# Kernel tuning notes

Measured on AMD Instinct MI355X. Metric: run time of the kernel, lower is better.

## Reference

```python
import jax, jax.numpy as jnp
import numpy as np

M, K, N, GROUP = 64, 4096, 11008, 128
NGROUPS = K // GROUP  # 32


def setup_inputs() -> dict:
    key = jax.random.key(0)
    k1, k2, k3, k4, k5 = jax.random.split(key, 5)
    x = jax.random.normal(k1, (M, K), dtype=jnp.float32)
    # packed int4 weights: 8 nibbles per int32, full 32-bit entropy
    qweight = jax.random.bits(k2, (K // 8, N), dtype=jnp.uint32).astype(jnp.int32)
    qzeros = jax.random.bits(k3, (NGROUPS, N // 8), dtype=jnp.uint32).astype(jnp.int32)
    scales = jax.random.uniform(k4, (NGROUPS, N), dtype=jnp.float32, minval=0.001, maxval=0.02)
    bias = jax.random.normal(k5, (N,), dtype=jnp.float32) * 0.01
    return {"x": x, "qweight": qweight, "qzeros": qzeros, "scales": scales, "bias": bias}


def dequantize(qweight, qzeros, scales):
    shifts = jnp.arange(8, dtype=jnp.int32) * 4  # nibble bit offsets 0..28
    # unpack weights: [K//8, N] -> [K//8, 8, N] -> [NGROUPS, GROUP, N]
    w = (jnp.right_shift(qweight[:, None, :], shifts[None, :, None]) & 15)
    w = w.reshape(-1, GROUP, qweight.shape[1])
    # unpack zeros: [NGROUPS, N//8] -> [NGROUPS, N//8, 8] -> [NGROUPS, 1, N]; GPTQ stores zero-1
    z = (jnp.right_shift(qzeros[:, :, None], shifts[None, None, :]) & 15) + 1
    z = z.reshape(z.shape[0], 1, -1)
    # scale * (q - zero), per group: [NGROUPS, GROUP, N] -> [K, N]
    W = scales[:, None, :] * (w - z).astype(scales.dtype)
    return W.reshape(-1, W.shape[2])


def reference(x, qweight, qzeros, scales, bias):
    W = dequantize(qweight, qzeros, scales)  # [K, N] fp32
    return jnp.matmul(x, W.astype(x.dtype)) + bias
```

## Files before the change

kernel.cpp:

```cpp
#include <hip/hip_runtime.h>
#include <hip/hip_bf16.h>

namespace {

constexpr int MM = 64;
constexpr int KK = 4096;
constexpr int NN = 11008;
constexpr int NZROW = NN / 8;
constexpr int BN = 128;
constexpr int KSPLIT = 8;
constexpr int KSEG = KK / KSPLIT;
constexpr int NTILES = NN / BN;
constexpr int BK = 32;
constexpr int NCH = KSEG / BK;
constexpr int GCH = 4;
constexpr int NG = NCH / GCH;
constexpr int AROWI = 68;
constexpr int ABUFI = MM * AROWI;
constexpr size_t WS_NEED = (size_t)KSPLIT * MM * NN * 4;

static_assert(NCH % GCH == 0, "groups must tile chunks");

typedef float f32x4 __attribute__((ext_vector_type(4)));
typedef short s16x8 __attribute__((ext_vector_type(8)));
typedef int   i32x4 __attribute__((ext_vector_type(4)));
typedef int   i32x2 __attribute__((ext_vector_type(2)));

__device__ __forceinline__ int pack_bf16(float a, float b) {
  union { __hip_bfloat162 h; int i; } u;
  u.h.x = __float2bfloat16(a);
  u.h.y = __float2bfloat16(b);
  return u.i;
}

__global__ __launch_bounds__(256) void prep_kernel(
    const float* __restrict__ bias, float* __restrict__ out)
{
  const int i = blockIdx.x * 256 + threadIdx.x;
  out[i] = bias[i % NN];
}

__global__ __launch_bounds__(256) void reduce_kernel(
    const float* __restrict__ ws, const float* __restrict__ bias,
    float* __restrict__ out)
{
  const int i4 = (blockIdx.x * 256 + threadIdx.x) * 4;
  f32x4 acc = *(const f32x4*)(bias + (i4 % NN));
  #pragma unroll
  for (int s = 0; s < KSPLIT; ++s)
    acc += *(const f32x4*)(ws + (size_t)s * (MM * NN) + i4);
  *(f32x4*)(out + i4) = acc;
}

template<bool ATOMIC>
__global__ __launch_bounds__(256, 4) void gptq_gemm_kernel(
    const float* __restrict__ x, const int* __restrict__ qw,
    const int* __restrict__ qz, const float* __restrict__ scales,
    float* __restrict__ out)
{
  __shared__ int As[2 * ABUFI];

  const int tid  = threadIdx.x;
  const int wave = tid >> 6;
  const int lane = tid & 63;
  const int c    = lane & 15;
  const int quad = lane >> 4;

  const int ks     = blockIdx.x & 7;
  const int ntile  = blockIdx.x >> 3;
  const int n0     = ntile * BN;
  const int kbase0 = ks * KSEG;
  const int grp0   = kbase0 >> 7;

  const int ncol = n0 + wave * 32 + c;

  const int arow0 = wave * 16 + (lane >> 5);
  const float* xp0 = x + (size_t)arow0 * KK + kbase0 + (lane & 31) * 4;

  const int* qwb = qw + ((size_t)(kbase0 >> 3) + quad) * NN + ncol;

  f32x4 acc[8];
  #pragma unroll
  for (int t = 0; t < 8; ++t) acc[t] = {0.f, 0.f, 0.f, 0.f};

  f32x4 S[8];
  int   pB0[4], pB1[4];
  float pS0[2], pS1[2];
  int   pZ0[2], pZ1[2];
  float s0, s1, C0, C1;

  auto stage_load = [&](int g) {
    const float* xp = xp0 + g * 128;
    #pragma unroll
    for (int j = 0; j < 8; ++j)
      S[j] = *(const f32x4*)(xp + (size_t)j * 2 * KK);
  };
  auto stage_write = [&](int g) {
    int* Ab = As + (g & 1) * ABUFI + arow0 * AROWI + (lane & 31) * 2;
    #pragma unroll
    for (int j = 0; j < 8; ++j) {
      i32x2 w2;
      w2.x = pack_bf16(S[j].x, S[j].y);
      w2.y = pack_bf16(S[j].z, S[j].w);
      *(i32x2*)&Ab[j * 2 * AROWI] = w2;
    }
  };
  auto pfB = [&](int i) {
    const int* qp = qwb + (size_t)i * 4 * NN;
    pB0[i & 3] = qp[0];
    pB1[i & 3] = qp[16];
  };
  auto pfS = [&](int g) {
    const int sl = g & 1;
    const float* sp = scales + (size_t)(grp0 + g) * NN + ncol;
    pS0[sl] = sp[0];
    pS1[sl] = sp[16];
    const int* zp = qz + (size_t)(grp0 + g) * NZROW + (ncol >> 3);
    pZ0[sl] = zp[0];
    pZ1[sl] = zp[2];
  };
  auto setSC = [&](int g) {
    const int sl = g & 1;
    const int sh = (ncol & 7) * 4;
    s0 = pS0[sl];
    s1 = pS1[sl];
    C0 = __int_as_float(0x4B000000 + ((pZ0[sl] >> sh) & 15) + 1);
    C1 = __int_as_float(0x4B000000 + ((pZ1[sl] >> sh) & 15) + 1);
  };
  auto dq8 = [&](int v, float s, float C) -> i32x4 {
    i32x4 p;
    p.x = pack_bf16(s * (__int_as_float(((v      ) & 15) | 0x4B000000) - C),
                    s * (__int_as_float(((v >>  4) & 15) | 0x4B000000) - C));
    p.y = pack_bf16(s * (__int_as_float(((v >>  8) & 15) | 0x4B000000) - C),
                    s * (__int_as_float(((v >> 12) & 15) | 0x4B000000) - C));
    p.z = pack_bf16(s * (__int_as_float(((v >> 16) & 15) | 0x4B000000) - C),
                    s * (__int_as_float(((v >> 20) & 15) | 0x4B000000) - C));
    p.w = pack_bf16(s * (__int_as_float(((v >> 24) & 15) | 0x4B000000) - C),
                    s * (__int_as_float(((v >> 28) & 15) | 0x4B000000) - C));
    return p;
  };

  pfS(0);
  stage_load(0);
  pfB(0); pfB(1); pfB(2);
  stage_write(0);
  __asm__ volatile("s_waitcnt lgkmcnt(0)\n\ts_barrier" ::: "memory");
  setSC(0);
  pfS(1);

  #pragma unroll
  for (int i = 0; i < NCH; ++i) {
    const int g = i >> 2, cc = i & 3, buf = g & 1;
    if (cc == 0 && g + 1 < NG) stage_load(g + 1);
    if (i + 3 < NCH) pfB(i + 3);

    union { i32x4 i4; s16x8 s8; } u0, u1;
    u0.i4 = dq8(pB0[i & 3], s0, C0);
    u1.i4 = dq8(pB1[i & 3], s1, C1);

    const int* Ab = As + buf * ABUFI;
    const int aoff = c * AROWI + cc * 16 + quad * 4;
    const s16x8 af0 = *(const s16x8*)&Ab[aoff];
    const s16x8 af1 = *(const s16x8*)&Ab[aoff + 16 * AROWI];
    const s16x8 af2 = *(const s16x8*)&Ab[aoff + 32 * AROWI];
    const s16x8 af3 = *(const s16x8*)&Ab[aoff + 48 * AROWI];

    acc[0] = __builtin_amdgcn_mfma_f32_16x16x32_bf16(af0, u0.s8, acc[0], 0, 0, 0);
    acc[1] = __builtin_amdgcn_mfma_f32_16x16x32_bf16(af0, u1.s8, acc[1], 0, 0, 0);
    acc[2] = __builtin_amdgcn_mfma_f32_16x16x32_bf16(af1, u0.s8, acc[2], 0, 0, 0);
    acc[3] = __builtin_amdgcn_mfma_f32_16x16x32_bf16(af1, u1.s8, acc[3], 0, 0, 0);
    acc[4] = __builtin_amdgcn_mfma_f32_16x16x32_bf16(af2, u0.s8, acc[4], 0, 0, 0);
    acc[5] = __builtin_amdgcn_mfma_f32_16x16x32_bf16(af2, u1.s8, acc[5], 0, 0, 0);
    acc[6] = __builtin_amdgcn_mfma_f32_16x16x32_bf16(af3, u0.s8, acc[6], 0, 0, 0);
    acc[7] = __builtin_amdgcn_mfma_f32_16x16x32_bf16(af3, u1.s8, acc[7], 0, 0, 0);

    if (cc == 3 && g + 1 < NG) {
      stage_write(g + 1);
      __asm__ volatile("s_waitcnt lgkmcnt(0)\n\ts_barrier" ::: "memory");
      setSC(g + 1);
      if (g + 2 < NG) pfS(g + 2);
    }
  }

  if (ATOMIC) {
    #pragma unroll
    for (int r = 0; r < 4; ++r) {
      #pragma unroll
      for (int t = 0; t < 2; ++t) {
        const f32x4 a = acc[r * 2 + t];
        float* op = out + (size_t)(r * 16 + quad * 4) * NN + ncol + t * 16;
        atomicAdd(&op[0],          a.x);
        atomicAdd(&op[NN],         a.y);
        atomicAdd(&op[2 * NN],     a.z);
        atomicAdd(&op[3 * NN],     a.w);
      }
    }
  } else {
    float* wsp = out + (size_t)ks * (MM * NN);
    #pragma unroll
    for (int r = 0; r < 4; ++r) {
      #pragma unroll
      for (int t = 0; t < 2; ++t) {
        const f32x4 a = acc[r * 2 + t];
        float* op = wsp + (size_t)(r * 16 + quad * 4) * NN + ncol + t * 16;
        op[0]      = a.x;
        op[NN]     = a.y;
        op[2 * NN] = a.z;
        op[3 * NN] = a.w;
      }
    }
  }
}

}

extern "C" void kernel_launch(void* const* d_in, const int* in_sizes, int n_in,
                              void* d_out, int out_size, void* d_ws, size_t ws_size,
                              hipStream_t stream) {
  const float* x      = (const float*)d_in[0];
  const int*   qw     = (const int*)d_in[1];
  const int*   qz     = (const int*)d_in[2];
  const float* scales = (const float*)d_in[3];
  const float* bias   = (const float*)d_in[4];
  float* out = (float*)d_out;

  if (ws_size >= WS_NEED) {
    float* ws = (float*)d_ws;
    gptq_gemm_kernel<false><<<NTILES * KSPLIT, 256, 0, stream>>>(x, qw, qz, scales, ws);
    reduce_kernel<<<(MM * NN) / 1024, 256, 0, stream>>>(ws, bias, out);
  } else {
    prep_kernel<<<(MM * NN) / 256, 256, 0, stream>>>(bias, out);
    gptq_gemm_kernel<true><<<NTILES * KSPLIT, 256, 0, stream>>>(x, qw, qz, scales, out);
  }
}
```

Before: 98.25 us.

## Pre-convert activations to bf16 and load A fragments directly from global memory

Adds a small pre-pass that converts x to bf16 into workspace, then the GEMM kernel drops its LDS staging of A (double buffer plus barriers) and loads each wave's A fragments straight from global/L2 with a one-chunk register prefetch. This removes the shared-memory round trip, the per-group barriers, and the redundant per-block fp32-to-bf16 conversion. In exchange it adds an extra kernel launch and more redundant global/L2 traffic, since every wave re-reads the full 64-row A tile. The workspace requirement also grows, so the fallback atomic path, which converts in-loop from fp32, may be taken if the workspace is too small.

```diff
diff --git a/kernel.cpp b/kernel.cpp
--- a/kernel.cpp
+++ b/kernel.cpp
@@ -13,24 +13,33 @@
 constexpr int NTILES = NN / BN;
 constexpr int BK = 32;
 constexpr int NCH = KSEG / BK;
-constexpr int GCH = 4;
-constexpr int NG = NCH / GCH;
-constexpr int AROWI = 68;
-constexpr int ABUFI = MM * AROWI;
-constexpr size_t WS_NEED = (size_t)KSPLIT * MM * NN * 4;
-
-static_assert(NCH % GCH == 0, "groups must tile chunks");
+constexpr int NG = 4;
+constexpr size_t XB_OFF_BYTES = (size_t)KSPLIT * MM * NN * 4;
+constexpr size_t WS_NEED = XB_OFF_BYTES + (size_t)MM * KK * 2;
 
 typedef float f32x4 __attribute__((ext_vector_type(4)));
 typedef short s16x8 __attribute__((ext_vector_type(8)));
 typedef int   i32x4 __attribute__((ext_vector_type(4)));
-typedef int   i32x2 __attribute__((ext_vector_type(2)));
 
 __device__ __forceinline__ int pack_bf16(float a, float b) {
   union { __hip_bfloat162 h; int i; } u;
   u.h.x = __float2bfloat16(a);
   u.h.y = __float2bfloat16(b);
   return u.i;
+}
+
+__global__ __launch_bounds__(256) void xcvt_kernel(
+    const float* __restrict__ x, unsigned short* __restrict__ xb)
+{
+  const int i8 = (blockIdx.x * 256 + threadIdx.x) * 8;
+  const f32x4 a = *(const f32x4*)(x + i8);
+  const f32x4 b = *(const f32x4*)(x + i8 + 4);
+  i32x4 p;
+  p.x = pack_bf16(a.x, a.y);
+  p.y = pack_bf16(a.z, a.w);
+  p.z = pack_bf16(b.x, b.y);
+  p.w = pack_bf16(b.z, b.w);
+  *(i32x4*)(xb + i8) = p;
 }
 
 __global__ __launch_bounds__(256) void prep_kernel(
@@ -52,14 +61,12 @@
   *(f32x4*)(out + i4) = acc;
 }
 
-template<bool ATOMIC>
+template<bool WS>
 __global__ __launch_bounds__(256, 4) void gptq_gemm_kernel(
     const float* __restrict__ x, const int* __restrict__ qw,
     const int* __restrict__ qz, const float* __restrict__ scales,
-    float* __restrict__ out)
-{
-  __shared__ int As[2 * ABUFI];
-
+    const unsigned short* __restrict__ xb, float* __restrict__ out)
+{
   const int tid  = threadIdx.x;
   const int wave = tid >> 6;
   const int lane = tid & 63;
@@ -74,36 +81,24 @@
 
   const int ncol = n0 + wave * 32 + c;
 
-  const int arow0 = wave * 16 + (lane >> 5);
-  const float* xp0 = x + (size_t)arow0 * KK + kbase0 + (lane & 31) * 4;
-
+  const unsigned short* xbb = xb + (size_t)c * KK + kbase0 + quad * 8;
   const int* qwb = qw + ((size_t)(kbase0 >> 3) + quad) * NN + ncol;
 
   f32x4 acc[8];
   #pragma unroll
   for (int t = 0; t < 8; ++t) acc[t] = {0.f, 0.f, 0.f, 0.f};
 
-  f32x4 S[8];
+  s16x8 pA[2][4];
   int   pB0[4], pB1[4];
   float pS0[2], pS1[2];
   int   pZ0[2], pZ1[2];
   float s0, s1, C0, C1;
 
-  auto stage_load = [&](int g) {
-    const float* xp = xp0 + g * 128;
-    #pragma unroll
-    for (int j = 0; j < 8; ++j)
-      S[j] = *(const f32x4*)(xp + (size_t)j * 2 * KK);
-  };
-  auto stage_write = [&](int g) {
-    int* Ab = As + (g & 1) * ABUFI + arow0 * AROWI + (lane & 31) * 2;
-    #pragma unroll
-    for (int j = 0; j < 8; ++j) {
-      i32x2 w2;
-      w2.x = pack_bf16(S[j].x, S[j].y);
-      w2.y = pack_bf16(S[j].z, S[j].w);
-      *(i32x2*)&Ab[j * 2 * AROWI] = w2;
-    }
+  auto ldA = [&](int i) {
+    const unsigned short* xp = xbb + i * BK;
+    #pragma unroll
+    for (int r = 0; r < 4; ++r)
+      pA[i & 1][r] = *(const s16x8*)(xp + (size_t)r * 16 * KK);
   };
   auto pfB = [&](int i) {
     const int* qp = qwb + (size_t)i * 4 * NN;
@@ -139,50 +134,61 @@
                     s * (__int_as_float(((v >> 28) & 15) | 0x4B000000) - C));
     return p;
   };
+  auto ldA_f32 = [&](int i, int r) -> s16x8 {
+    const float* xa = x + (size_t)(r * 16 + c) * KK + kbase0 + i * BK + quad * 8;
+    const f32x4 a0 = *(const f32x4*)xa;
+    const f32x4 a1 = *(const f32x4*)(xa + 4);
+    union { i32x4 i4; s16x8 s8; } ua;
+    ua.i4.x = pack_bf16(a0.x, a0.y);
+    ua.i4.y = pack_bf16(a0.z, a0.w);
+    ua.i4.z = pack_bf16(a1.x, a1.y);
+    ua.i4.w = pack_bf16(a1.z, a1.w);
+    return ua.s8;
+  };
 
   pfS(0);
-  stage_load(0);
   pfB(0); pfB(1); pfB(2);
-  stage_write(0);
-  __asm__ volatile("s_waitcnt lgkmcnt(0)\n\ts_barrier" ::: "memory");
+  if (WS) ldA(0);
   setSC(0);
   pfS(1);
 
   #pragma unroll
   for (int i = 0; i < NCH; ++i) {
-    const int g = i >> 2, cc = i & 3, buf = g & 1;
-    if (cc == 0 && g + 1 < NG) stage_load(g + 1);
     if (i + 3 < NCH) pfB(i + 3);
+    if (WS && i + 1 < NCH) ldA(i + 1);
 
     union { i32x4 i4; s16x8 s8; } u0, u1;
     u0.i4 = dq8(pB0[i & 3], s0, C0);
     u1.i4 = dq8(pB1[i & 3], s1, C1);
 
-    const int* Ab = As + buf * ABUFI;
-    const int aoff = c * AROWI + cc * 16 + quad * 4;
-    const s16x8 af0 = *(const s16x8*)&Ab[aoff];
-    const s16x8 af1 = *(const s16x8*)&Ab[aoff + 16 * AROWI];
-    const s16x8 af2 = *(const s16x8*)&Ab[aoff + 32 * AROWI];
-    const s16x8 af3 = *(const s16x8*)&Ab[aoff + 48 * AROWI];
-
-    acc[0] = __builtin_amdgcn_mfma_f32_16x16x32_bf16(af0, u0.s8, acc[0], 0, 0, 0);
-    acc[1] = __builtin_amdgcn_mfma_f32_16x16x32_bf16(af0, u1.s8, acc[1], 0, 0, 0);
-    acc[2] = __builtin_amdgcn_mfma_f32_16x16x32_bf16(af1, u0.s8, acc[2], 0, 0, 0);
-    acc[3] = __builtin_amdgcn_mfma_f32_16x16x32_bf16(af1, u1.s8, acc[3], 0, 0, 0);
-    acc[4] = __builtin_amdgcn_mfma_f32_16x16x32_bf16(af2, u0.s8, acc[4], 0, 0, 0);
-    acc[5] = __builtin_amdgcn_mfma_f32_16x16x32_bf16(af2, u1.s8, acc[5], 0, 0, 0);
-    acc[6] = __builtin_amdgcn_mfma_f32_16x16x32_bf16(af3, u0.s8, acc[6], 0, 0, 0);
-    acc[7] = __builtin_amdgcn_mfma_f32_16x16x32_bf16(af3, u1.s8, acc[7], 0, 0, 0);
-
-    if (cc == 3 && g + 1 < NG) {
-      stage_write(g + 1);
-      __asm__ volatile("s_waitcnt lgkmcnt(0)\n\ts_barrier" ::: "memory");
-      setSC(g + 1);
-      if (g + 2 < NG) pfS(g + 2);
+    #pragma unroll
+    for (int r = 0; r < 4; ++r) {
+      const s16x8 af = WS ? pA[i & 1][r] : ldA_f32(i, r);
+      acc[r * 2 + 0] = __builtin_amdgcn_mfma_f32_16x16x32_bf16(af, u0.s8, acc[r * 2 + 0], 0, 0, 0);
+      acc[r * 2 + 1] = __builtin_amdgcn_mfma_f32_16x16x32_bf16(af, u1.s8, acc[r * 2 + 1], 0, 0, 0);
+    }
+
+    if ((i & 3) == 3) {
+      const int g = i >> 2;
+      if (g + 1 < NG) { setSC(g + 1); if (g + 2 < NG) pfS(g + 2); }
     }
   }
 
-  if (ATOMIC) {
+  if (WS) {
+    float* wsp = out + (size_t)ks * (MM * NN);
+    #pragma unroll
+    for (int r = 0; r < 4; ++r) {
+      #pragma unroll
+      for (int t = 0; t < 2; ++t) {
+        const f32x4 a = acc[r * 2 + t];
+        float* op = wsp + (size_t)(r * 16 + quad * 4) * NN + ncol + t * 16;
+        op[0]      = a.x;
+        op[NN]     = a.y;
+        op[2 * NN] = a.z;
+        op[3 * NN] = a.w;
+      }
+    }
+  } else {
     #pragma unroll
     for (int r = 0; r < 4; ++r) {
       #pragma unroll
@@ -195,20 +201,6 @@
         atomicAdd(&op[3 * NN],     a.w);
       }
     }
-  } else {
-    float* wsp = out + (size_t)ks * (MM * NN);
-    #pragma unroll
-    for (int r = 0; r < 4; ++r) {
-      #pragma unroll
-      for (int t = 0; t < 2; ++t) {
-        const f32x4 a = acc[r * 2 + t];
-        float* op = wsp + (size_t)(r * 16 + quad * 4) * NN + ncol + t * 16;
-        op[0]      = a.x;
-        op[NN]     = a.y;
-        op[2 * NN] = a.z;
-        op[3 * NN] = a.w;
-      }
-    }
   }
 }
 
@@ -226,10 +218,12 @@
 
   if (ws_size >= WS_NEED) {
     float* ws = (float*)d_ws;
-    gptq_gemm_kernel<false><<<NTILES * KSPLIT, 256, 0, stream>>>(x, qw, qz, scales, ws);
+    unsigned short* xb = (unsigned short*)((char*)d_ws + XB_OFF_BYTES);
+    xcvt_kernel<<<(MM * KK) / 2048, 256, 0, stream>>>(x, xb);
+    gptq_gemm_kernel<true><<<NTILES * KSPLIT, 256, 0, stream>>>(x, qw, qz, scales, xb, ws);
     reduce_kernel<<<(MM * NN) / 1024, 256, 0, stream>>>(ws, bias, out);
   } else {
     prep_kernel<<<(MM * NN) / 256, 256, 0, stream>>>(bias, out);
-    gptq_gemm_kernel<true><<<NTILES * KSPLIT, 256, 0, stream>>>(x, qw, qz, scales, out);
+    gptq_gemm_kernel<false><<<NTILES * KSPLIT, 256, 0, stream>>>(x, qw, qz, scales, nullptr, out);
   }
 }
```

Result: slower. 108.5 us (+10.5%).
